# Performance work log

Hardware: AMD Instinct MI355X
Metric: run time of the kernel (lower is better)

The kernel has to match this reference:

```python
import jax, jax.numpy as jnp
import numpy as np

D_IN = 1024   # input_channels
N_H = 2048    # madden
K = 4         # num_slices (low-rank k)
N_CLS = 1000
BATCH = 8192
BN_EPS = 1e-5


def hmu_quad(x, mu, lam, v):
    """quad[b,n] = lam[n]*||x-mu_n||^2 + sum_k ((x-mu_n).v_{n,k})^2.
    Algebraically identical to einsum('bni,nij,bnj->bn', diff, lam*I + V^T V, diff)
    without materializing the (n,d,d) Hessian or (b,n,d) diff tensor.
    x: (b,d), mu: (n,d), lam: (n,), v: (n,k,d) -> (b,n)
    """
    xsq = jnp.sum(x * x, axis=-1, keepdims=True)          # (b,1)
    msq = jnp.sum(mu * mu, axis=-1)                        # (n,)
    sqdist = xsq - 2.0 * (x @ mu.T) + msq                  # (b,n)
    proj = jnp.einsum('bd,nkd->bnk', x, v) - jnp.einsum('nd,nkd->nk', mu, v)  # (b,n,k)
    return lam * sqdist + jnp.sum(proj * proj, axis=-1)


def batchnorm(x, gamma, beta):
    # BatchNorm1d in training mode: batch mean, biased variance
    m = jnp.mean(x, axis=0)
    var = jnp.mean((x - m) ** 2, axis=0)
    return (x - m) * jax.lax.rsqrt(var + BN_EPS) * gamma + beta


def setup_inputs() -> dict:
    key = jax.random.key(0)
    ks = jax.random.split(key, 12)
    return {
        'x': jax.random.normal(ks[0], (BATCH, D_IN), dtype=jnp.float32),
        'mu1': jax.random.uniform(ks[1], (N_H, D_IN), dtype=jnp.float32),
        'lam1': jax.random.uniform(ks[2], (N_H,), dtype=jnp.float32) * 0.01,
        'v1': jax.random.normal(ks[3], (N_H, K, D_IN), dtype=jnp.float32) / np.sqrt(D_IN),
        'g1': jnp.ones((N_H,), jnp.float32),
        'b1': jnp.zeros((N_H,), jnp.float32),
        'mu2': jax.random.uniform(ks[4], (N_H, N_H), dtype=jnp.float32),
        'lam2': jax.random.uniform(ks[5], (N_H,), dtype=jnp.float32) * 0.01,
        'v2': jax.random.normal(ks[6], (N_H, K, N_H), dtype=jnp.float32) / np.sqrt(N_H),
        'g2': jnp.ones((N_H,), jnp.float32),
        'b2': jnp.zeros((N_H,), jnp.float32),
        'Wl': jax.random.normal(ks[7], (N_CLS, N_H), dtype=jnp.float32) / np.sqrt(N_H),
        'bl': jnp.zeros((N_CLS,), jnp.float32),
    }


def reference(x, mu1, lam1, v1, g1, b1, mu2, lam2, v2, g2, b2, Wl, bl):
    # hmu1 (Type='no_exp'): out = -quad
    out = -hmu_quad(x, mu1, lam1, v1)
    feat1 = batchnorm(out, g1, b1)                 # (b, N_H)
    # hmu2 (Type='exp'): out = exp(-quad / d), d = N_H
    out = jnp.exp(-hmu_quad(feat1, mu2, lam2, v2) / N_H)
    feat2 = jax.nn.relu(batchnorm(out, g2, b2))    # (b, N_H)
    logits = feat2 @ Wl.T + bl                     # (b, N_CLS)
    return logits, (feat1, feat2, feat2)
```

## Files before the change

kernel.cpp:

```cpp
#include <hip/hip_runtime.h>
#include <hip/hip_bf16.h>

typedef __attribute__((ext_vector_type(8))) short bf16x8;
typedef __attribute__((ext_vector_type(4))) float f32x4;

#define BATCH 8192
#define D_IN 1024
#define N_H 2048
#define N_CLS 1000
#define BN_EPS 1e-5f

__device__ __forceinline__ f32x4 zero4() { f32x4 z; z.x = 0.f; z.y = 0.f; z.z = 0.f; z.w = 0.f; return z; }

__device__ __forceinline__ unsigned short f2b(float x) {
    unsigned u = __float_as_uint(x);
    u += 0x7fff + ((u >> 16) & 1);
    return (unsigned short)(u >> 16);
}

__device__ __forceinline__ ushort4 f2b4(float4 f) {
    ushort4 o; o.x = f2b(f.x); o.y = f2b(f.y); o.z = f2b(f.z); o.w = f2b(f.w); return o;
}

__device__ __forceinline__ void async16(const void* g, void* l) {
    __builtin_amdgcn_global_load_lds((const __attribute__((address_space(1))) void*)g,
                                     (__attribute__((address_space(3))) void*)l, 16, 0, 0);
}

__global__ void cvt_wl(const float4* __restrict__ in, ushort4* __restrict__ out) {
    long i = (long)blockIdx.x * 256 + threadIdx.x;
    int j = (int)(i >> 9);
    ushort4 o; o.x = 0; o.y = 0; o.z = 0; o.w = 0;
    if (j < N_CLS) o = f2b4(in[i]);
    out[i] = o;
}

__device__ __forceinline__ float block_sum(float v, float* red) {
    #pragma unroll
    for (int off = 32; off > 0; off >>= 1) v += __shfl_down(v, off);
    __syncthreads();
    if ((threadIdx.x & 63) == 0) red[threadIdx.x >> 6] = v;
    __syncthreads();
    return red[0] + red[1] + red[2] + red[3];
}

__global__ void prep_nv(const float4* __restrict__ mu, const float4* __restrict__ v,
                        ushort4* __restrict__ mu_bf, ushort4* __restrict__ v_bf,
                        float* __restrict__ msq, float* __restrict__ c, int D4) {
    __shared__ float red[4];
    int n = blockIdx.x, tid = threadIdx.x;
    const float4* m = mu + (long)n * D4;
    const float4* vv = v + (long)n * 4 * D4;
    ushort4* mb = mu_bf + (long)n * D4;
    ushort4* vb = v_bf + (long)n * 4 * D4;
    float sm = 0, s0 = 0, s1 = 0, s2 = 0, s3 = 0;
    for (int d = tid; d < D4; d += 256) {
        float4 mm = m[d];
        mb[d] = f2b4(mm);
        sm += mm.x * mm.x + mm.y * mm.y + mm.z * mm.z + mm.w * mm.w;
        float4 w0 = vv[d], w1 = vv[D4 + d], w2 = vv[2 * D4 + d], w3 = vv[3 * D4 + d];
        vb[d] = f2b4(w0); vb[D4 + d] = f2b4(w1); vb[2 * D4 + d] = f2b4(w2); vb[3 * D4 + d] = f2b4(w3);
        s0 += mm.x * w0.x + mm.y * w0.y + mm.z * w0.z + mm.w * w0.w;
        s1 += mm.x * w1.x + mm.y * w1.y + mm.z * w1.z + mm.w * w1.w;
        s2 += mm.x * w2.x + mm.y * w2.y + mm.z * w2.z + mm.w * w2.w;
        s3 += mm.x * w3.x + mm.y * w3.y + mm.z * w3.z + mm.w * w3.w;
    }
    float r;
    r = block_sum(sm, red); if (tid == 0) msq[n] = r;
    r = block_sum(s0, red); if (tid == 0) c[n * 4 + 0] = r;
    r = block_sum(s1, red); if (tid == 0) c[n * 4 + 1] = r;
    r = block_sum(s2, red); if (tid == 0) c[n * 4 + 2] = r;
    r = block_sum(s3, red); if (tid == 0) c[n * 4 + 3] = r;
}

__global__ void prep_x(const float4* __restrict__ X, ushort4* __restrict__ Xbf,
                       float* __restrict__ out, int D4) {
    __shared__ float red[4];
    int b = blockIdx.x, tid = threadIdx.x;
    const float4* row = X + (long)b * D4;
    ushort4* rb = Xbf + (long)b * D4;
    float s = 0;
    for (int d = tid; d < D4; d += 256) {
        float4 f = row[d];
        rb[d] = f2b4(f);
        s += f.x * f.x + f.y * f.y + f.z * f.z + f.w * f.w;
    }
    float r = block_sum(s, red);
    if (tid == 0) out[b] = r;
}

__global__ void bn_finalize(const double* __restrict__ sums, const double* __restrict__ sumsq,
                            const float* __restrict__ g, const float* __restrict__ b,
                            float* __restrict__ scale, float* __restrict__ shift) {
    int c = blockIdx.x * 256 + threadIdx.x;
    double m = sums[c] * (1.0 / BATCH);
    double var = sumsq[c] * (1.0 / BATCH) - m * m;
    float inv = (float)(1.0 / sqrt(var + (double)BN_EPS));
    float sc = g[c] * inv;
    scale[c] = sc;
    shift[c] = b[c] - (float)m * sc;
}

__global__ void bn_apply1(float4* __restrict__ X, ushort4* __restrict__ Xbf,
                          float* __restrict__ fsq, const float4* __restrict__ scale,
                          const float4* __restrict__ shift) {
    __shared__ float red[4];
    int b = blockIdx.x, tid = threadIdx.x;
    float4* row = X + (long)b * (N_H / 4);
    ushort4* rb = Xbf + (long)b * (N_H / 4);
    float s = 0;
    for (int c = tid; c < N_H / 4; c += 256) {
        float4 xv = row[c], sc = scale[c], sh = shift[c];
        float4 y;
        y.x = xv.x * sc.x + sh.x; y.y = xv.y * sc.y + sh.y;
        y.z = xv.z * sc.z + sh.z; y.w = xv.w * sc.w + sh.w;
        row[c] = y;
        rb[c] = f2b4(y);
        s += y.x * y.x + y.y * y.y + y.z * y.z + y.w * y.w;
    }
    float r = block_sum(s, red);
    if (tid == 0) fsq[b] = r;
}

__global__ void bn_apply2(float4* __restrict__ X, float4* __restrict__ X2,
                          ushort4* __restrict__ Xbf,
                          const float4* __restrict__ scale, const float4* __restrict__ shift) {
    int b = blockIdx.x, tid = threadIdx.x;
    float4* row = X + (long)b * (N_H / 4);
    float4* row2 = X2 + (long)b * (N_H / 4);
    ushort4* rb = Xbf + (long)b * (N_H / 4);
    for (int c = tid; c < N_H / 4; c += 256) {
        float4 xv = row[c], sc = scale[c], sh = shift[c];
        float4 y;
        y.x = fmaxf(xv.x * sc.x + sh.x, 0.f); y.y = fmaxf(xv.y * sc.y + sh.y, 0.f);
        y.z = fmaxf(xv.z * sc.z + sh.z, 0.f); y.w = fmaxf(xv.w * sc.w + sh.w, 0.f);
        row[c] = y;
        row2[c] = y;
        rb[c] = f2b4(y);
    }
}

__device__ __forceinline__ void gemm_tile(const short* __restrict__ A, const short* __restrict__ B,
                                          int K, short* As, short* Bs, f32x4 acc[4][4]) {
    const int tid = threadIdx.x;
    const int lane = tid & 63, wave = tid >> 6;
    const int wm = wave & 1, wn = wave >> 1;
    const int lr = lane & 15, lq = lane >> 4;

    const short* ga[4]; const short* gb[4];
    short* la[4]; short* lb[4];
    #pragma unroll
    for (int p = 0; p < 4; ++p) {
        int c = tid + 256 * p;
        int row = c >> 3, slot = c & 7;
        int g = slot ^ (row & 7);
        ga[p] = A + (long)row * K + g * 8;
        gb[p] = B + (long)row * K + g * 8;
        la[p] = As + c * 8;
        lb[p] = Bs + c * 8;
    }

    const int s0 = (lq ^ (lr & 7)) * 8;
    const short* paBase = As + (wm * 64 + lr) * 64;
    const short* pbBase = Bs + (wn * 64 + lr) * 64;

    for (int kt = 0; kt < K; kt += 64) {
        #pragma unroll
        for (int p = 0; p < 4; ++p) async16(ga[p], la[p]);
        #pragma unroll
        for (int p = 0; p < 4; ++p) async16(gb[p], lb[p]);
        #pragma unroll
        for (int p = 0; p < 4; ++p) { ga[p] += 64; gb[p] += 64; }
        __syncthreads();
        #pragma unroll
        for (int ks = 0; ks < 2; ++ks) {
            const int so = s0 ^ (ks * 32);
            bf16x8 af[4], bfr[4];
            #pragma unroll
            for (int i = 0; i < 4; i++) {
                af[i]  = *(const bf16x8*)(paBase + i * 1024 + so);
                bfr[i] = *(const bf16x8*)(pbBase + i * 1024 + so);
            }
            #pragma unroll
            for (int i = 0; i < 4; i++)
                #pragma unroll
                for (int j = 0; j < 4; j++)
                    acc[i][j] = __builtin_amdgcn_mfma_f32_16x16x32_bf16(af[i], bfr[j], acc[i][j], 0, 0, 0);
        }
        __syncthreads();
    }
}

__global__ __launch_bounds__(256) void gemm_s(const short* __restrict__ A, const short* __restrict__ B,
                                              float* __restrict__ quadS, const float* __restrict__ rsq,
                                              const float* __restrict__ msq, const float* __restrict__ lam,
                                              int K, int N) {
    __shared__ short As[128 * 64];
    __shared__ short Bs[128 * 64];
    int m0 = blockIdx.y * 128, n0 = blockIdx.x * 128;
    f32x4 acc[4][4];
    #pragma unroll
    for (int i = 0; i < 4; i++)
        #pragma unroll
        for (int j = 0; j < 4; j++) acc[i][j] = zero4();
    gemm_tile(A + (long)m0 * K, B + (long)n0 * K, K, As, Bs, acc);

    const int lane = threadIdx.x & 63, wave = threadIdx.x >> 6;
    const int wm = wave & 1, wn = wave >> 1, lr = lane & 15, lq = lane >> 4;
    #pragma unroll
    for (int j = 0; j < 4; j++) {
        int col = n0 + wn * 64 + j * 16 + lr;
        float lamc = lam[col], msqc = msq[col];
        #pragma unroll
        for (int i = 0; i < 4; i++) {
            int rowb = m0 + wm * 64 + i * 16 + lq * 4;
            #pragma unroll
            for (int r = 0; r < 4; r++) {
                int row = rowb + r;
                quadS[(long)row * N + col] = lamc * (rsq[row] - 2.0f * acc[i][j][r] + msqc);
            }
        }
    }
}

template <int DO_EXP>
__global__ __launch_bounds__(256) void gemm_p(const short* __restrict__ A, const short* __restrict__ B,
                                              const float* __restrict__ quadS, const float* __restrict__ cvec,
                                              float* __restrict__ out, double* __restrict__ sums,
                                              double* __restrict__ sumsq, int K) {
    __shared__ short As[128 * 64];
    __shared__ short Bs[128 * 64];
    int m0 = blockIdx.y * 128, n0 = blockIdx.x * 128;
    f32x4 acc[4][4];
    #pragma unroll
    for (int i = 0; i < 4; i++)
        #pragma unroll
        for (int j = 0; j < 4; j++) acc[i][j] = zero4();
    gemm_tile(A + (long)m0 * K, B + (long)n0 * K, K, As, Bs, acc);

    const int lane = threadIdx.x & 63, wave = threadIdx.x >> 6;
    const int wm = wave & 1, wn = wave >> 1, lr = lane & 15, lq = lane >> 4;
    #pragma unroll
    for (int j = 0; j < 4; j++) {
        int col = n0 + wn * 64 + j * 16 + lr;
        float cc = cvec[col];
        double lsum = 0.0, lsq = 0.0;
        int n = col >> 2;
        #pragma unroll
        for (int i = 0; i < 4; i++) {
            int rowb = m0 + wm * 64 + i * 16 + lq * 4;
            #pragma unroll
            for (int r = 0; r < 4; r++) {
                float d = acc[i][j][r] - cc;
                float s = d * d;
                s += __shfl_xor(s, 1);
                s += __shfl_xor(s, 2);
                if ((lane & 3) == 0) {
                    int row = rowb + r;
                    float q = quadS[(long)row * N_H + n] + s;
                    float val = DO_EXP ? __expf(-q * (1.0f / 2048.0f)) : -q;
                    out[(long)row * N_H + n] = val;
                    lsum += val;
                    lsq += (double)val * val;
                }
            }
        }
        lsum += __shfl_xor(lsum, 16); lsum += __shfl_xor(lsum, 32);
        lsq  += __shfl_xor(lsq, 16);  lsq  += __shfl_xor(lsq, 32);
        if (lane < 16 && (lane & 3) == 0) {
            atomicAdd(&sums[n], lsum);
            atomicAdd(&sumsq[n], lsq);
        }
    }
}

__global__ __launch_bounds__(256) void gemm_lin(const short* __restrict__ A, const short* __restrict__ B,
                                                const float* __restrict__ bias, float* __restrict__ out,
                                                int K) {
    __shared__ short As[128 * 64];
    __shared__ short Bs[128 * 64];
    int m0 = blockIdx.y * 128, n0 = blockIdx.x * 128;
    f32x4 acc[4][4];
    #pragma unroll
    for (int i = 0; i < 4; i++)
        #pragma unroll
        for (int j = 0; j < 4; j++) acc[i][j] = zero4();
    gemm_tile(A + (long)m0 * K, B + (long)n0 * K, K, As, Bs, acc);

    const int lane = threadIdx.x & 63, wave = threadIdx.x >> 6;
    const int wm = wave & 1, wn = wave >> 1, lr = lane & 15, lq = lane >> 4;
    #pragma unroll
    for (int j = 0; j < 4; j++) {
        int col = n0 + wn * 64 + j * 16 + lr;
        float bb = (col < N_CLS) ? bias[col] : 0.f;
        #pragma unroll
        for (int i = 0; i < 4; i++) {
            int rowb = m0 + wm * 64 + i * 16 + lq * 4;
            #pragma unroll
            for (int r = 0; r < 4; r++) {
                if (col < N_CLS) {
                    int row = rowb + r;
                    out[(long)row * N_CLS + col] = acc[i][j][r] + bb;
                }
            }
        }
    }
}

extern "C" void kernel_launch(void* const* d_in, const int* in_sizes, int n_in,
                              void* d_out, int out_size, void* d_ws, size_t ws_size,
                              hipStream_t stream) {
    const float* x   = (const float*)d_in[0];
    const float* mu1 = (const float*)d_in[1];
    const float* lam1= (const float*)d_in[2];
    const float* v1  = (const float*)d_in[3];
    const float* g1  = (const float*)d_in[4];
    const float* b1  = (const float*)d_in[5];
    const float* mu2 = (const float*)d_in[6];
    const float* lam2= (const float*)d_in[7];
    const float* v2  = (const float*)d_in[8];
    const float* g2  = (const float*)d_in[9];
    const float* b2  = (const float*)d_in[10];
    const float* Wl  = (const float*)d_in[11];
    const float* bl  = (const float*)d_in[12];

    float* out = (float*)d_out;
    float* logits = out;
    float* feat1  = out + (long)BATCH * N_CLS;
    float* feat2a = feat1 + (long)BATCH * N_H;
    float* feat2b = feat2a + (long)BATCH * N_H;
    float* quadS  = feat2b;

    char* w = (char*)d_ws;
    size_t off = 0;
    auto alloc = [&](size_t bytes) -> void* {
        void* p = w + off;
        off += (bytes + 255) & ~(size_t)255;
        return p;
    };
    const size_t SZ_XBF  = (size_t)BATCH * D_IN * 2;
    const size_t SZ_MU1  = (size_t)N_H * D_IN * 2;
    const size_t SZ_V1   = (size_t)N_H * 4 * D_IN * 2;
    const size_t SZ_MU2  = (size_t)N_H * N_H * 2;
    const size_t SZ_V2   = (size_t)N_H * 4 * N_H * 2;

    char* regionA = (char*)alloc(SZ_XBF + SZ_MU1 + SZ_V1);
    char* regionB = (char*)alloc(SZ_MU2 + SZ_V2);
    short* x_bf   = (short*)(regionA);
    short* mu1_bf = (short*)(regionA + SZ_XBF);
    short* v1_bf  = (short*)(regionA + SZ_XBF + SZ_MU1);
    short* f1_bf  = (short*)(regionA);
    short* mu2_bf = (short*)(regionB);
    short* v2_bf  = (short*)(regionB + SZ_MU2);
    short* f2_bf  = (short*)(regionB);
    short* wl_bf  = (short*)alloc((size_t)1024 * N_H * 2);
    float* xsq    = (float*)alloc(BATCH * 4);
    float* fsq    = (float*)alloc(BATCH * 4);
    float* msq1   = (float*)alloc(N_H * 4);
    float* c1     = (float*)alloc(N_H * 4 * 4);
    float* msq2   = (float*)alloc(N_H * 4);
    float* c2     = (float*)alloc(N_H * 4 * 4);
    double* sums1 = (double*)alloc(N_H * 8 * 4);
    double* sumsq1 = sums1 + N_H;
    double* sums2  = sums1 + 2 * N_H;
    double* sumsq2 = sums1 + 3 * N_H;
    float* scale1 = (float*)alloc(N_H * 4);
    float* shift1 = (float*)alloc(N_H * 4);
    float* scale2 = (float*)alloc(N_H * 4);
    float* shift2 = (float*)alloc(N_H * 4);

    (void)in_sizes; (void)n_in; (void)out_size; (void)ws_size;

    hipMemsetAsync(sums1, 0, N_H * 8 * 4, stream);
    prep_x<<<BATCH, 256, 0, stream>>>((const float4*)x, (ushort4*)x_bf, xsq, D_IN / 4);
    prep_nv<<<N_H, 256, 0, stream>>>((const float4*)mu1, (const float4*)v1, (ushort4*)mu1_bf, (ushort4*)v1_bf, msq1, c1, D_IN / 4);
    prep_nv<<<N_H, 256, 0, stream>>>((const float4*)mu2, (const float4*)v2, (ushort4*)mu2_bf, (ushort4*)v2_bf, msq2, c2, N_H / 4);
    cvt_wl<<<(1024 * (N_H / 4)) / 256, 256, 0, stream>>>((const float4*)Wl, (ushort4*)wl_bf);

    gemm_s<<<dim3(N_H / 128, BATCH / 128), 256, 0, stream>>>(x_bf, mu1_bf, quadS, xsq, msq1, lam1, D_IN, N_H);
    gemm_p<0><<<dim3((N_H * 4) / 128, BATCH / 128), 256, 0, stream>>>(x_bf, v1_bf, quadS, c1, feat1, sums1, sumsq1, D_IN);

    bn_finalize<<<N_H / 256, 256, 0, stream>>>(sums1, sumsq1, g1, b1, scale1, shift1);
    bn_apply1<<<BATCH, 256, 0, stream>>>((float4*)feat1, (ushort4*)f1_bf, fsq, (const float4*)scale1, (const float4*)shift1);

    gemm_s<<<dim3(N_H / 128, BATCH / 128), 256, 0, stream>>>(f1_bf, mu2_bf, quadS, fsq, msq2, lam2, N_H, N_H);
    gemm_p<1><<<dim3((N_H * 4) / 128, BATCH / 128), 256, 0, stream>>>(f1_bf, v2_bf, quadS, c2, feat2a, sums2, sumsq2, N_H);

    bn_finalize<<<N_H / 256, 256, 0, stream>>>(sums2, sumsq2, g2, b2, scale2, shift2);
    bn_apply2<<<BATCH, 256, 0, stream>>>((float4*)feat2a, (float4*)feat2b, (ushort4*)f2_bf, (const float4*)scale2, (const float4*)shift2);

    gemm_lin<<<dim3(1024 / 128, BATCH / 128), 256, 0, stream>>>(f2_bf, wl_bf, bl, logits, N_H);
}
```

Measured before the change: 1.355 ms.

## Double-buffer GEMM LDS tiles to overlap async loads with MFMA compute

Replaces the single-buffered load/sync/compute/sync loop in the shared GEMM tile routine with a two-stage ping-pong over two LDS buffers. The next K-slice is issued with async copies while MFMAs run on the current one, which also cuts the loop to one barrier per slice. It also raises wave priority around the MFMA block. LDS use per block doubles to 64 KB, which can lower occupancy, and the unrolled schedule assumes K/64 is even and at least 2.

```diff
diff --git a/kernel.cpp b/kernel.cpp
--- a/kernel.cpp
+++ b/kernel.cpp
@@ -141,14 +141,19 @@
 }
 
 __device__ __forceinline__ void gemm_tile(const short* __restrict__ A, const short* __restrict__ B,
-                                          int K, short* As, short* Bs, f32x4 acc[4][4]) {
+                                          int K, f32x4 acc[4][4]) {
+    __shared__ short As0[128 * 64];
+    __shared__ short Bs0[128 * 64];
+    __shared__ short As1[128 * 64];
+    __shared__ short Bs1[128 * 64];
+
     const int tid = threadIdx.x;
-    const int lane = tid & 63, wave = tid >> 6;
-    const int wm = wave & 1, wn = wave >> 1;
+    const int lane = tid & 63;
+    const int wm = (tid >> 6) & 1, wn = tid >> 7;
     const int lr = lane & 15, lq = lane >> 4;
 
     const short* ga[4]; const short* gb[4];
-    short* la[4]; short* lb[4];
+    int lo[4];
     #pragma unroll
     for (int p = 0; p < 4; ++p) {
         int c = tid + 256 * p;
@@ -156,54 +161,68 @@
         int g = slot ^ (row & 7);
         ga[p] = A + (long)row * K + g * 8;
         gb[p] = B + (long)row * K + g * 8;
-        la[p] = As + c * 8;
-        lb[p] = Bs + c * 8;
-    }
-
+        lo[p] = c * 8;
+    }
     const int s0 = (lq ^ (lr & 7)) * 8;
-    const short* paBase = As + (wm * 64 + lr) * 64;
-    const short* pbBase = Bs + (wn * 64 + lr) * 64;
-
-    for (int kt = 0; kt < K; kt += 64) {
-        #pragma unroll
-        for (int p = 0; p < 4; ++p) async16(ga[p], la[p]);
-        #pragma unroll
-        for (int p = 0; p < 4; ++p) async16(gb[p], lb[p]);
+
+    auto stage = [&](short* Asb, short* Bsb) {
+        #pragma unroll
+        for (int p = 0; p < 4; ++p) async16(ga[p], Asb + lo[p]);
+        #pragma unroll
+        for (int p = 0; p < 4; ++p) async16(gb[p], Bsb + lo[p]);
         #pragma unroll
         for (int p = 0; p < 4; ++p) { ga[p] += 64; gb[p] += 64; }
-        __syncthreads();
+    };
+    auto compute = [&](const short* Asb, const short* Bsb) {
+        const short* pa = Asb + (wm * 64 + lr) * 64;
+        const short* pb = Bsb + (wn * 64 + lr) * 64;
         #pragma unroll
         for (int ks = 0; ks < 2; ++ks) {
             const int so = s0 ^ (ks * 32);
             bf16x8 af[4], bfr[4];
             #pragma unroll
             for (int i = 0; i < 4; i++) {
-                af[i]  = *(const bf16x8*)(paBase + i * 1024 + so);
-                bfr[i] = *(const bf16x8*)(pbBase + i * 1024 + so);
+                af[i]  = *(const bf16x8*)(pa + i * 1024 + so);
+                bfr[i] = *(const bf16x8*)(pb + i * 1024 + so);
             }
+            __builtin_amdgcn_s_setprio(1);
             #pragma unroll
             for (int i = 0; i < 4; i++)
                 #pragma unroll
                 for (int j = 0; j < 4; j++)
                     acc[i][j] = __builtin_amdgcn_mfma_f32_16x16x32_bf16(af[i], bfr[j], acc[i][j], 0, 0, 0);
+            __builtin_amdgcn_s_setprio(0);
         }
+    };
+
+    const int NT = K >> 6;
+    stage(As0, Bs0);
+    __syncthreads();
+    for (int t = 0; t < NT / 2 - 1; ++t) {
+        stage(As1, Bs1);
+        compute(As0, Bs0);
         __syncthreads();
-    }
+        stage(As0, Bs0);
+        compute(As1, Bs1);
+        __syncthreads();
+    }
+    stage(As1, Bs1);
+    compute(As0, Bs0);
+    __syncthreads();
+    compute(As1, Bs1);
 }
 
 __global__ __launch_bounds__(256) void gemm_s(const short* __restrict__ A, const short* __restrict__ B,
                                               float* __restrict__ quadS, const float* __restrict__ rsq,
                                               const float* __restrict__ msq, const float* __restrict__ lam,
                                               int K, int N) {
-    __shared__ short As[128 * 64];
-    __shared__ short Bs[128 * 64];
     int m0 = blockIdx.y * 128, n0 = blockIdx.x * 128;
     f32x4 acc[4][4];
     #pragma unroll
     for (int i = 0; i < 4; i++)
         #pragma unroll
         for (int j = 0; j < 4; j++) acc[i][j] = zero4();
-    gemm_tile(A + (long)m0 * K, B + (long)n0 * K, K, As, Bs, acc);
+    gemm_tile(A + (long)m0 * K, B + (long)n0 * K, K, acc);
 
     const int lane = threadIdx.x & 63, wave = threadIdx.x >> 6;
     const int wm = wave & 1, wn = wave >> 1, lr = lane & 15, lq = lane >> 4;
@@ -228,15 +247,13 @@
                                               const float* __restrict__ quadS, const float* __restrict__ cvec,
                                               float* __restrict__ out, double* __restrict__ sums,
                                               double* __restrict__ sumsq, int K) {
-    __shared__ short As[128 * 64];
-    __shared__ short Bs[128 * 64];
     int m0 = blockIdx.y * 128, n0 = blockIdx.x * 128;
     f32x4 acc[4][4];
     #pragma unroll
     for (int i = 0; i < 4; i++)
         #pragma unroll
         for (int j = 0; j < 4; j++) acc[i][j] = zero4();
-    gemm_tile(A + (long)m0 * K, B + (long)n0 * K, K, As, Bs, acc);
+    gemm_tile(A + (long)m0 * K, B + (long)n0 * K, K, acc);
 
     const int lane = threadIdx.x & 63, wave = threadIdx.x >> 6;
     const int wm = wave & 1, wn = wave >> 1, lr = lane & 15, lq = lane >> 4;
@@ -277,15 +294,13 @@
 __global__ __launch_bounds__(256) void gemm_lin(const short* __restrict__ A, const short* __restrict__ B,
                                                 const float* __restrict__ bias, float* __restrict__ out,
                                                 int K) {
-    __shared__ short As[128 * 64];
-    __shared__ short Bs[128 * 64];
     int m0 = blockIdx.y * 128, n0 = blockIdx.x * 128;
     f32x4 acc[4][4];
     #pragma unroll
     for (int i = 0; i < 4; i++)
         #pragma unroll
         for (int j = 0; j < 4; j++) acc[i][j] = zero4();
-    gemm_tile(A + (long)m0 * K, B + (long)n0 * K, K, As, Bs, acc);
+    gemm_tile(A + (long)m0 * K, B + (long)n0 * K, K, acc);
 
     const int lane = threadIdx.x & 63, wave = threadIdx.x >> 6;
     const int wm = wave & 1, wn = wave >> 1, lr = lane & 15, lq = lane >> 4;
```

Measured after the change: 1.210 ms. -10.7%, faster.
